# Kernel tuning notes

Measured on AMD Instinct MI355X. Metric: run time of the kernel, lower is better.

## Reference

```python
import jax, jax.numpy as jnp
import numpy as np

DIM = 1024
NUM_HEADS = 16
HEAD_DIM = DIM // NUM_HEADS


def setup_inputs() -> dict:
    key = jax.random.key(0)
    ks = jax.random.split(key, 6)
    B, N, C = 2, 2048, DIM
    s = 1.0 / np.sqrt(C)
    return {
        "x": jax.random.normal(ks[0], (B, N, C), dtype=jnp.float32),
        "Wq": jax.random.normal(ks[1], (C, C), dtype=jnp.float32) * s,
        "Wk": jax.random.normal(ks[2], (C, C), dtype=jnp.float32) * s,
        "Wv": jax.random.normal(ks[3], (C, C), dtype=jnp.float32) * s,
        "Wproj": jax.random.normal(ks[4], (C, C), dtype=jnp.float32) * s,
        "bproj": jax.random.normal(ks[5], (C,), dtype=jnp.float32) * 0.01,
    }


def reference(x, Wq, Wk, Wv, Wproj, bproj):
    B, N, C = x.shape
    H, D = NUM_HEADS, HEAD_DIM
    scale = D ** -0.5
    # Linear (torch convention: y = x @ W.T), then split heads -> [B, H, N, D]
    q = (x @ Wq.T).reshape(B, N, H, D).transpose(0, 2, 1, 3)
    k = (x @ Wk.T).reshape(B, N, H, D).transpose(0, 2, 1, 3)
    v = (x @ Wv.T).reshape(B, N, H, D).transpose(0, 2, 1, 3)
    attn = jnp.einsum("bhnd,bhmd->bhnm", q, k) * scale  # [B,H,N,N]
    attn = jax.nn.softmax(attn, axis=-1)
    out = jnp.einsum("bhnm,bhmd->bhnd", attn, v)  # [B,H,N,D]
    out = out.transpose(0, 2, 1, 3).reshape(B, N, C)
    return out @ Wproj.T + bproj
```

## Files before the change

kernel.cpp:

```cpp
#include <hip/hip_runtime.h>
#include <stdint.h>

typedef unsigned short u16;
typedef unsigned int u32;

typedef __bf16 bf16x8 __attribute__((ext_vector_type(8)));
typedef float f32x4 __attribute__((ext_vector_type(4)));

#define LOG2E_SCALE 0.18033688011112042f

static __device__ __forceinline__ u16 f2bf(float f) {
  union { float f; u32 u; } v; v.f = f;
  u32 r = v.u + 0x7fffu + ((v.u >> 16) & 1u);
  return (u16)(r >> 16);
}
static __device__ __forceinline__ u32 pk2(float a, float b) {
  u32 r;
  asm("v_cvt_pk_bf16_f32 %0, %1, %2" : "=v"(r) : "v"(a), "v"(b));
  return r;
}
static __device__ __forceinline__ float fexp2(float x) {
  return __builtin_amdgcn_exp2f(x);
}
static __device__ __forceinline__ float blo(u32 u) {
  union { u32 u; float f; } v; v.u = u << 16; return v.f;
}
static __device__ __forceinline__ float bhi(u32 u) {
  union { u32 u; float f; } v; v.u = u & 0xffff0000u; return v.f;
}

static __device__ __forceinline__ void gl_lds16(const void* g, void* l) {
  __builtin_amdgcn_global_load_lds(
      (const __attribute__((address_space(1))) u32*)g,
      (__attribute__((address_space(3))) u32*)l, 16, 0, 0);
}

__global__ void cast_kernel(const float* __restrict__ x, const float* __restrict__ wq,
                            const float* __restrict__ wk, const float* __restrict__ wv,
                            const float* __restrict__ wp,
                            u16* __restrict__ xb, u16* __restrict__ wqb, u16* __restrict__ wkb,
                            u16* __restrict__ wvb, u16* __restrict__ wpb) {
  const float* src; u16* dst; int n;
  switch (blockIdx.y) {
    case 0: src = x;  dst = xb;  n = 4194304; break;
    case 1: src = wq; dst = wqb; n = 1048576; break;
    case 2: src = wk; dst = wkb; n = 1048576; break;
    case 3: src = wv; dst = wvb; n = 1048576; break;
    default: src = wp; dst = wpb; n = 1048576; break;
  }
  int i = (blockIdx.x * 256 + threadIdx.x) * 8;
  if (i >= n) return;
  float4 a = *(const float4*)(src + i);
  float4 b = *(const float4*)(src + i + 4);
  uint4 o;
  o.x = pk2(a.x, a.y); o.y = pk2(a.z, a.w);
  o.z = pk2(b.x, b.y); o.w = pk2(b.z, b.w);
  *(uint4*)(dst + i) = o;
}

__global__ __launch_bounds__(256, 3) void gemm_qkv(
    const u16* __restrict__ A, const u16* __restrict__ Bq, const u16* __restrict__ Bk,
    const u16* __restrict__ Bv, u16* __restrict__ oQ, u16* __restrict__ oK,
    u16* __restrict__ oVt)
{
  constexpr int K = 1024;
  __shared__ u16 As[128 * 32];
  __shared__ u16 Bs[128 * 32];
  __shared__ float tbuf[4][16 * 68];

  const int tid  = threadIdx.x;
  const int lane = tid & 63;
  const int wave = tid >> 6;
  const int cl   = lane & 15;
  const int g    = lane >> 4;
  const int wm   = (wave >> 1) * 64;
  const int wn   = (wave & 1) * 64;
  const int bm   = blockIdx.y * 128;
  const int bn   = blockIdx.x * 128;
  const int z    = blockIdx.z;
  const u16* B = (z == 0 ? Bq : (z == 1 ? Bk : Bv));

  f32x4 zero4 = {0.f, 0.f, 0.f, 0.f};
  f32x4 acc[4][4];
#pragma unroll
  for (int i = 0; i < 4; i++)
#pragma unroll
    for (int j = 0; j < 4; j++) acc[i][j] = zero4;

  const int srow = tid >> 2;
  const int sch  = (tid & 3) ^ ((srow >> 1) & 3);
  const char* aG = (const char*)(A + (size_t)(bm + srow) * K) + sch * 16;
  const char* bG = (const char*)(B + (size_t)(bn + srow) * K) + sch * 16;
  char* aL = (char*)As + tid * 16;
  char* bL = (char*)Bs + tid * 16;
  const size_t rstep = (size_t)64 * K * 2;

  const int swz = (cl >> 1) & 3;

  for (int k0 = 0; k0 < K; k0 += 32) {
    gl_lds16(aG + k0 * 2, aL);
    gl_lds16(aG + rstep + k0 * 2, aL + 4096);
    gl_lds16(bG + k0 * 2, bL);
    gl_lds16(bG + rstep + k0 * 2, bL + 4096);
    __syncthreads();

    bf16x8 af[4], bf[4];
#pragma unroll
    for (int i = 0; i < 4; i++)
      af[i] = *(const bf16x8*)(As + (wm + i * 16 + cl) * 32 + ((g ^ swz) & 3) * 8);
#pragma unroll
    for (int j = 0; j < 4; j++)
      bf[j] = *(const bf16x8*)(Bs + (wn + j * 16 + cl) * 32 + ((g ^ swz) & 3) * 8);
#pragma unroll
    for (int i = 0; i < 4; i++)
#pragma unroll
      for (int j = 0; j < 4; j++)
        acc[i][j] = __builtin_amdgcn_mfma_f32_16x16x32_bf16(af[i], bf[j], acc[i][j], 0, 0, 0);
    __syncthreads();
  }

  const int rq = g * 4;
  if (z <= 1) {
    u16* o = z ? oK : oQ;
    const float cs = z ? 1.0f : LOG2E_SCALE;
#pragma unroll
    for (int i = 0; i < 4; i++)
#pragma unroll
      for (int j = 0; j < 4; j++)
#pragma unroll
        for (int r = 0; r < 4; r++) {
          int gm = bm + wm + i * 16 + rq + r;
          int gn = bn + wn + j * 16 + cl;
          int b = gm >> 11, ns = gm & 2047;
          int h = gn >> 6,  d  = gn & 63;
          o[(((size_t)(b * 16 + h)) * 2048 + ns) * 64 + d] = f2bf(acc[i][j][r] * cs);
        }
  } else {
    float* tb = tbuf[wave];
#pragma unroll
    for (int j = 0; j < 4; j++) {
      asm volatile("s_waitcnt lgkmcnt(0)" ::: "memory");
#pragma unroll
      for (int i = 0; i < 4; i++)
        *(f32x4*)(tb + cl * 68 + i * 16 + rq) = acc[i][j];
      asm volatile("s_waitcnt lgkmcnt(0)" ::: "memory");
#pragma unroll
      for (int half = 0; half < 2; half++) {
        int dd = lane >> 2, p = (lane & 3) + half * 4;
        f32x4 x0 = *(const f32x4*)(tb + dd * 68 + p * 8);
        f32x4 x1 = *(const f32x4*)(tb + dd * 68 + p * 8 + 4);
        uint4 pkd;
        pkd.x = pk2(x0[0], x0[1]); pkd.y = pk2(x0[2], x0[3]);
        pkd.z = pk2(x1[0], x1[1]); pkd.w = pk2(x1[2], x1[3]);
        int gn = bn + wn + j * 16 + dd;
        int gm = bm + wm + p * 8;
        int b = gm >> 11, nn = gm & 2047;
        int h = gn >> 6,  dl = gn & 63;
        *(uint4*)(oVt + (((size_t)(b * 16 + h)) * 64 + dl) * 2048 + nn) = pkd;
      }
    }
  }
}

__global__ __launch_bounds__(512, 6) void attn_kernel(
    const u16* __restrict__ Q, const u16* __restrict__ Km,
    const u16* __restrict__ Vt, u16* __restrict__ Op, float* __restrict__ lp)
{
  __shared__ u16 ks[2][64 * 64];
  __shared__ u16 vs[2][64 * 64];
  __shared__ u16 ps[128 * 36];

  const int tid  = threadIdx.x;
  const int lane = tid & 63;
  const int W    = tid >> 6;
  const int cl   = lane & 15;
  const int g    = lane >> 4;
  const int bh   = blockIdx.x;
  const int qt   = blockIdx.y;
  const int sp   = blockIdx.z;

  const char* kS = (const char*)Km + (size_t)bh * 2048 * 128 + (size_t)sp * 1024 * 128;
  const char* vS = (const char*)Vt + (size_t)bh * 64 * 4096 + (size_t)sp * 2048;

  const u16* qbase = Q + ((size_t)bh * 2048 + qt * 128 + W * 16) * 64;
  bf16x8 qf[2];
#pragma unroll
  for (int h = 0; h < 2; h++)
    qf[h] = *(const bf16x8*)(qbase + cl * 64 + h * 32 + g * 8);

  auto stage_k = [&](int t) {
    const char* kT = kS + (size_t)t * 8192;
    int kv = tid >> 3, s = tid & 7;
    gl_lds16(kT + kv * 128 + (((s ^ kv) & 7) * 16), (char*)ks[t & 1] + tid * 16);
  };
  auto stage_v = [&](int t) {
    const char* vT = vS + (size_t)t * 128;
    int d = tid >> 3, s = tid & 7;
    gl_lds16(vT + (size_t)d * 4096 + (((s ^ d) & 7) * 16), (char*)vs[t & 1] + tid * 16);
  };

  stage_k(0);
  stage_v(0);

  f32x4 zero4 = {0.f, 0.f, 0.f, 0.f};
  f32x4 o_acc[4];
#pragma unroll
  for (int j = 0; j < 4; j++) o_acc[j] = zero4;
  float li = 0.f;

  for (int t = 0; t < 16; ++t) {
    __syncthreads();
    if (t < 15) { stage_k(t + 1); stage_v(t + 1); }

    const u16* kb = ks[t & 1];
    const u16* vb = vs[t & 1];

    f32x4 st[4];
#pragma unroll
    for (int j = 0; j < 4; j++) st[j] = zero4;
#pragma unroll
    for (int h = 0; h < 2; h++) {
#pragma unroll
      for (int j = 0; j < 4; j++) {
        bf16x8 kf = *(const bf16x8*)(kb + (j * 16 + cl) * 64 + (((h * 4 + g) ^ (cl & 7)) & 7) * 8);
        st[j] = __builtin_amdgcn_mfma_f32_16x16x32_bf16(kf, qf[h], st[j], 0, 0, 0);
      }
    }

#pragma unroll
    for (int j = 0; j < 4; j++)
#pragma unroll
      for (int r = 0; r < 4; r++) {
        float p = fexp2(st[j][r]);
        st[j][r] = p;
        li += p;
      }

    char* prow = (char*)ps + (W * 16 + cl) * 72;
#pragma unroll
    for (int h32 = 0; h32 < 2; h32++) {
#pragma unroll
      for (int jj = 0; jj < 2; jj++) {
        int j = h32 * 2 + jj;
        uint2 w;
        w.x = pk2(st[j][0], st[j][1]);
        w.y = pk2(st[j][2], st[j][3]);
        *(uint2*)(prow + jj * 32 + g * 8) = w;
      }
      bf16x8 pf, vf[4];
      union { bf16x8 v; uint2 u[2]; } pu;
      pu.u[0] = *(const uint2*)(prow + g * 16);
      pu.u[1] = *(const uint2*)(prow + g * 16 + 8);
      pf = pu.v;
#pragma unroll
      for (int j = 0; j < 4; j++)
        vf[j] = *(const bf16x8*)(vb + (j * 16 + cl) * 64 + (((h32 * 4 + g) ^ (cl & 7)) & 7) * 8);
#pragma unroll
      for (int j = 0; j < 4; j++)
        o_acc[j] = __builtin_amdgcn_mfma_f32_16x16x32_bf16(pf, vf[j], o_acc[j], 0, 0, 0);
    }
  }

  li += __shfl_xor(li, 16, 64);
  li += __shfl_xor(li, 32, 64);
  const int b = bh >> 4, hh = bh & 15;
  u16* Os = Op + (size_t)sp * 4194304;
  float* ls = lp + sp * 65536;
  if (g == 0) ls[bh * 2048 + qt * 128 + W * 16 + cl] = li;
#pragma unroll
  for (int r = 0; r < 4; r++) {
    int row = qt * 128 + W * 16 + g * 4 + r;
    u16* orow = Os + ((size_t)b * 2048 + row) * 1024 + hh * 64;
#pragma unroll
    for (int j = 0; j < 4; j++)
      orow[j * 16 + cl] = f2bf(o_acc[j][r]);
  }
}

__global__ void reduce_o(const u16* __restrict__ Op, const float* __restrict__ lp,
                         u16* __restrict__ Ow) {
  int t = blockIdx.x * 256 + threadIdx.x;
  int idx = t * 8;
  int b   = idx >> 21;
  int rem = idx & 2097151;
  int row = rem >> 10;
  int h   = (rem & 1023) >> 6;
  int lidx = (b * 16 + h) * 2048 + row;
  float inv = 1.0f / (lp[lidx] + lp[65536 + lidx]);
  uint4 a = *(const uint4*)(Op + idx);
  uint4 c = *(const uint4*)(Op + 4194304 + idx);
  uint4 o;
  o.x = pk2((blo(a.x) + blo(c.x)) * inv, (bhi(a.x) + bhi(c.x)) * inv);
  o.y = pk2((blo(a.y) + blo(c.y)) * inv, (bhi(a.y) + bhi(c.y)) * inv);
  o.z = pk2((blo(a.z) + blo(c.z)) * inv, (bhi(a.z) + bhi(c.z)) * inv);
  o.w = pk2((blo(a.w) + blo(c.w)) * inv, (bhi(a.w) + bhi(c.w)) * inv);
  *(uint4*)(Ow + idx) = o;
}

__global__ __launch_bounds__(256, 4) void proj_gemm(
    const u16* __restrict__ A, const u16* __restrict__ B,
    float* __restrict__ out, const float* __restrict__ bias)
{
  constexpr int K = 1024;
  __shared__ u16 As[64 * 32];
  __shared__ u16 Bs[128 * 32];

  const int tid  = threadIdx.x;
  const int lane = tid & 63;
  const int wave = tid >> 6;
  const int cl   = lane & 15;
  const int g    = lane >> 4;
  const int wm   = (wave >> 1) * 32;
  const int wn   = (wave & 1) * 64;
  const int bm   = blockIdx.y * 64;
  const int bn   = blockIdx.x * 128;

  f32x4 zero4 = {0.f, 0.f, 0.f, 0.f};
  f32x4 acc[2][4];
#pragma unroll
  for (int i = 0; i < 2; i++)
#pragma unroll
    for (int j = 0; j < 4; j++) acc[i][j] = zero4;

  const int srow = tid >> 2;
  const int sch  = (tid & 3) ^ ((srow >> 1) & 3);
  const char* aG = (const char*)(A + (size_t)(bm + srow) * K) + sch * 16;
  const char* bG = (const char*)(B + (size_t)(bn + srow) * K) + sch * 16;
  char* aL = (char*)As + tid * 16;
  char* bL = (char*)Bs + tid * 16;
  const size_t rstep = (size_t)64 * K * 2;

  const int swz = (cl >> 1) & 3;

  for (int k0 = 0; k0 < K; k0 += 32) {
    gl_lds16(aG + k0 * 2, aL);
    gl_lds16(bG + k0 * 2, bL);
    gl_lds16(bG + rstep + k0 * 2, bL + 4096);
    __syncthreads();

    bf16x8 af[2], bf[4];
#pragma unroll
    for (int i = 0; i < 2; i++)
      af[i] = *(const bf16x8*)(As + (wm + i * 16 + cl) * 32 + ((g ^ swz) & 3) * 8);
#pragma unroll
    for (int j = 0; j < 4; j++)
      bf[j] = *(const bf16x8*)(Bs + (wn + j * 16 + cl) * 32 + ((g ^ swz) & 3) * 8);
#pragma unroll
    for (int i = 0; i < 2; i++)
#pragma unroll
      for (int j = 0; j < 4; j++)
        acc[i][j] = __builtin_amdgcn_mfma_f32_16x16x32_bf16(af[i], bf[j], acc[i][j], 0, 0, 0);
    __syncthreads();
  }

  const int rq = g * 4;
#pragma unroll
  for (int i = 0; i < 2; i++)
#pragma unroll
    for (int j = 0; j < 4; j++)
#pragma unroll
      for (int r = 0; r < 4; r++) {
        int gm = bm + wm + i * 16 + rq + r;
        int gn = bn + wn + j * 16 + cl;
        out[(size_t)gm * 1024 + gn] = acc[i][j][r] + bias[gn];
      }
}

extern "C" void kernel_launch(void* const* d_in, const int* in_sizes, int n_in,
                              void* d_out, int out_size, void* d_ws, size_t ws_size,
                              hipStream_t stream) {
  const float* x     = (const float*)d_in[0];
  const float* Wq    = (const float*)d_in[1];
  const float* Wk    = (const float*)d_in[2];
  const float* Wv    = (const float*)d_in[3];
  const float* Wp    = (const float*)d_in[4];
  const float* bproj = (const float*)d_in[5];

  u16* ws  = (u16*)d_ws;
  u16* xb  = ws;
  u16* wqb = xb + 4194304;
  u16* wkb = wqb + 1048576;
  u16* wvb = wkb + 1048576;
  u16* wpb = wvb + 1048576;
  u16* Qw  = wpb + 1048576;
  u16* Kw  = Qw + 4194304;
  u16* Vw  = Kw + 4194304;
  u16* Ow  = Vw + 4194304;
  u16* Opart = Ow + 4194304;
  float* lpart = (float*)(Opart + 8388608);
  (void)in_sizes; (void)n_in; (void)out_size; (void)ws_size;

  cast_kernel<<<dim3(2048, 5), 256, 0, stream>>>(x, Wq, Wk, Wv, Wp, xb, wqb, wkb, wvb, wpb);
  gemm_qkv<<<dim3(8, 32, 3), 256, 0, stream>>>(xb, wqb, wkb, wvb, Qw, Kw, Vw);
  attn_kernel<<<dim3(32, 16, 2), 512, 0, stream>>>(Qw, Kw, Vw, Opart, lpart);
  reduce_o<<<dim3(2048), 256, 0, stream>>>(Opart, lpart, Ow);
  proj_gemm<<<dim3(8, 64), 256, 0, stream>>>(Ow, wpb, (float*)d_out, bproj);
}
```

Measured before the change: 183.9 us.

## Fuse split-KV reduction into projection GEMM, double-buffer GEMMs, MFMA row sums

The reduce_o kernel is removed. The projection GEMM now loads both partial attention outputs plus their row sums while staging its A tile, and writes the normalized bf16 tile to LDS itself. This drops one launch and an intermediate round trip through memory. Both GEMMs get double-buffered LDS staging with one barrier per iteration, and the attention kernel computes row sums with an extra MFMA against a ones vector instead of scalar adds and shuffles. The cast kernel launch is compacted to remove idle blocks. The cost is that the partial reduction is recomputed by each of the 8 column blocks, and the A loads become register-routed rather than direct-to-LDS.

```diff
diff --git a/kernel.cpp b/kernel.cpp
--- a/kernel.cpp
+++ b/kernel.cpp
@@ -40,16 +40,21 @@
                             const float* __restrict__ wp,
                             u16* __restrict__ xb, u16* __restrict__ wqb, u16* __restrict__ wkb,
                             u16* __restrict__ wvb, u16* __restrict__ wpb) {
-  const float* src; u16* dst; int n;
-  switch (blockIdx.y) {
-    case 0: src = x;  dst = xb;  n = 4194304; break;
-    case 1: src = wq; dst = wqb; n = 1048576; break;
-    case 2: src = wk; dst = wkb; n = 1048576; break;
-    case 3: src = wv; dst = wvb; n = 1048576; break;
-    default: src = wp; dst = wpb; n = 1048576; break;
-  }
-  int i = (blockIdx.x * 256 + threadIdx.x) * 8;
-  if (i >= n) return;
+  int id = blockIdx.x;
+  const float* src; u16* dst; int local;
+  if (id < 2048) {
+    src = x; dst = xb; local = id;
+  } else {
+    int w = (id - 2048) >> 9;
+    local = (id - 2048) & 511;
+    switch (w) {
+      case 0: src = wq; dst = wqb; break;
+      case 1: src = wk; dst = wkb; break;
+      case 2: src = wv; dst = wvb; break;
+      default: src = wp; dst = wpb; break;
+    }
+  }
+  int i = (local * 256 + threadIdx.x) * 8;
   float4 a = *(const float4*)(src + i);
   float4 b = *(const float4*)(src + i + 4);
   uint4 o;
@@ -64,9 +69,7 @@
     u16* __restrict__ oVt)
 {
   constexpr int K = 1024;
-  __shared__ u16 As[128 * 32];
-  __shared__ u16 Bs[128 * 32];
-  __shared__ float tbuf[4][16 * 68];
+  __shared__ u16 smem[2][2][128 * 32];
 
   const int tid  = threadIdx.x;
   const int lane = tid & 63;
@@ -91,32 +94,39 @@
   const int sch  = (tid & 3) ^ ((srow >> 1) & 3);
   const char* aG = (const char*)(A + (size_t)(bm + srow) * K) + sch * 16;
   const char* bG = (const char*)(B + (size_t)(bn + srow) * K) + sch * 16;
-  char* aL = (char*)As + tid * 16;
-  char* bL = (char*)Bs + tid * 16;
   const size_t rstep = (size_t)64 * K * 2;
 
+  auto stage = [&](int it) {
+    char* aL = (char*)smem[it & 1][0] + tid * 16;
+    char* bL = (char*)smem[it & 1][1] + tid * 16;
+    gl_lds16(aG + it * 64, aL);
+    gl_lds16(aG + it * 64 + rstep, aL + 4096);
+    gl_lds16(bG + it * 64, bL);
+    gl_lds16(bG + it * 64 + rstep, bL + 4096);
+  };
+
+  stage(0);
+
   const int swz = (cl >> 1) & 3;
 
-  for (int k0 = 0; k0 < K; k0 += 32) {
-    gl_lds16(aG + k0 * 2, aL);
-    gl_lds16(aG + rstep + k0 * 2, aL + 4096);
-    gl_lds16(bG + k0 * 2, bL);
-    gl_lds16(bG + rstep + k0 * 2, bL + 4096);
+  for (int it = 0; it < 32; ++it) {
     __syncthreads();
-
+    if (it < 31) stage(it + 1);
+
+    const u16* as = smem[it & 1][0];
+    const u16* bs = smem[it & 1][1];
     bf16x8 af[4], bf[4];
 #pragma unroll
     for (int i = 0; i < 4; i++)
-      af[i] = *(const bf16x8*)(As + (wm + i * 16 + cl) * 32 + ((g ^ swz) & 3) * 8);
+      af[i] = *(const bf16x8*)(as + (wm + i * 16 + cl) * 32 + ((g ^ swz) & 3) * 8);
 #pragma unroll
     for (int j = 0; j < 4; j++)
-      bf[j] = *(const bf16x8*)(Bs + (wn + j * 16 + cl) * 32 + ((g ^ swz) & 3) * 8);
+      bf[j] = *(const bf16x8*)(bs + (wn + j * 16 + cl) * 32 + ((g ^ swz) & 3) * 8);
 #pragma unroll
     for (int i = 0; i < 4; i++)
 #pragma unroll
       for (int j = 0; j < 4; j++)
         acc[i][j] = __builtin_amdgcn_mfma_f32_16x16x32_bf16(af[i], bf[j], acc[i][j], 0, 0, 0);
-    __syncthreads();
   }
 
   const int rq = g * 4;
@@ -136,7 +146,8 @@
           o[(((size_t)(b * 16 + h)) * 2048 + ns) * 64 + d] = f2bf(acc[i][j][r] * cs);
         }
   } else {
-    float* tb = tbuf[wave];
+    __syncthreads();
+    float* tb = (float*)smem + wave * (16 * 68);
 #pragma unroll
     for (int j = 0; j < 4; j++) {
       asm volatile("s_waitcnt lgkmcnt(0)" ::: "memory");
@@ -188,6 +199,11 @@
   for (int h = 0; h < 2; h++)
     qf[h] = *(const bf16x8*)(qbase + cl * 64 + h * 32 + g * 8);
 
+  union { bf16x8 v; u32 u[4]; } onesu;
+#pragma unroll
+  for (int k = 0; k < 4; k++) onesu.u[k] = 0x3f803f80u;
+  const bf16x8 onesf = onesu.v;
+
   auto stage_k = [&](int t) {
     const char* kT = kS + (size_t)t * 8192;
     int kv = tid >> 3, s = tid & 7;
@@ -206,7 +222,7 @@
   f32x4 o_acc[4];
 #pragma unroll
   for (int j = 0; j < 4; j++) o_acc[j] = zero4;
-  float li = 0.f;
+  f32x4 l_acc = zero4;
 
   for (int t = 0; t < 16; ++t) {
     __syncthreads();
@@ -230,11 +246,8 @@
 #pragma unroll
     for (int j = 0; j < 4; j++)
 #pragma unroll
-      for (int r = 0; r < 4; r++) {
-        float p = fexp2(st[j][r]);
-        st[j][r] = p;
-        li += p;
-      }
+      for (int r = 0; r < 4; r++)
+        st[j][r] = fexp2(st[j][r]);
 
     char* prow = (char*)ps + (W * 16 + cl) * 72;
 #pragma unroll
@@ -258,15 +271,18 @@
 #pragma unroll
       for (int j = 0; j < 4; j++)
         o_acc[j] = __builtin_amdgcn_mfma_f32_16x16x32_bf16(pf, vf[j], o_acc[j], 0, 0, 0);
+      l_acc = __builtin_amdgcn_mfma_f32_16x16x32_bf16(pf, onesf, l_acc, 0, 0, 0);
     }
   }
 
-  li += __shfl_xor(li, 16, 64);
-  li += __shfl_xor(li, 32, 64);
   const int b = bh >> 4, hh = bh & 15;
   u16* Os = Op + (size_t)sp * 4194304;
   float* ls = lp + sp * 65536;
-  if (g == 0) ls[bh * 2048 + qt * 128 + W * 16 + cl] = li;
+  if (cl == 0) {
+#pragma unroll
+    for (int r = 0; r < 4; r++)
+      ls[bh * 2048 + qt * 128 + W * 16 + g * 4 + r] = l_acc[r];
+  }
 #pragma unroll
   for (int r = 0; r < 4; r++) {
     int row = qt * 128 + W * 16 + g * 4 + r;
@@ -277,33 +293,13 @@
   }
 }
 
-__global__ void reduce_o(const u16* __restrict__ Op, const float* __restrict__ lp,
-                         u16* __restrict__ Ow) {
-  int t = blockIdx.x * 256 + threadIdx.x;
-  int idx = t * 8;
-  int b   = idx >> 21;
-  int rem = idx & 2097151;
-  int row = rem >> 10;
-  int h   = (rem & 1023) >> 6;
-  int lidx = (b * 16 + h) * 2048 + row;
-  float inv = 1.0f / (lp[lidx] + lp[65536 + lidx]);
-  uint4 a = *(const uint4*)(Op + idx);
-  uint4 c = *(const uint4*)(Op + 4194304 + idx);
-  uint4 o;
-  o.x = pk2((blo(a.x) + blo(c.x)) * inv, (bhi(a.x) + bhi(c.x)) * inv);
-  o.y = pk2((blo(a.y) + blo(c.y)) * inv, (bhi(a.y) + bhi(c.y)) * inv);
-  o.z = pk2((blo(a.z) + blo(c.z)) * inv, (bhi(a.z) + bhi(c.z)) * inv);
-  o.w = pk2((blo(a.w) + blo(c.w)) * inv, (bhi(a.w) + bhi(c.w)) * inv);
-  *(uint4*)(Ow + idx) = o;
-}
-
 __global__ __launch_bounds__(256, 4) void proj_gemm(
-    const u16* __restrict__ A, const u16* __restrict__ B,
-    float* __restrict__ out, const float* __restrict__ bias)
+    const u16* __restrict__ Op, const float* __restrict__ lp,
+    const u16* __restrict__ B, float* __restrict__ out, const float* __restrict__ bias)
 {
   constexpr int K = 1024;
-  __shared__ u16 As[64 * 32];
-  __shared__ u16 Bs[128 * 32];
+  __shared__ u16 As[2][64 * 32];
+  __shared__ u16 Bs[2][128 * 32];
 
   const int tid  = threadIdx.x;
   const int lane = tid & 63;
@@ -324,33 +320,51 @@
 
   const int srow = tid >> 2;
   const int sch  = (tid & 3) ^ ((srow >> 1) & 3);
-  const char* aG = (const char*)(A + (size_t)(bm + srow) * K) + sch * 16;
+  const int gmA  = bm + srow;
+  const int bA   = gmA >> 11, rowA = gmA & 2047;
+  const u16* aBase = Op + (size_t)gmA * 1024 + sch * 8;
   const char* bG = (const char*)(B + (size_t)(bn + srow) * K) + sch * 16;
-  char* aL = (char*)As + tid * 16;
-  char* bL = (char*)Bs + tid * 16;
   const size_t rstep = (size_t)64 * K * 2;
 
+  auto stage = [&](int it) {
+    char* bL = (char*)Bs[it & 1] + tid * 16;
+    gl_lds16(bG + it * 64, bL);
+    gl_lds16(bG + it * 64 + rstep, bL + 4096);
+    int col = it * 32 + sch * 8;
+    int lidx = (bA * 16 + (col >> 6)) * 2048 + rowA;
+    float inv = 1.0f / (lp[lidx] + lp[65536 + lidx]);
+    uint4 a0 = *(const uint4*)(aBase + it * 32);
+    uint4 a1 = *(const uint4*)(aBase + it * 32 + 4194304);
+    uint4 o;
+    o.x = pk2((blo(a0.x) + blo(a1.x)) * inv, (bhi(a0.x) + bhi(a1.x)) * inv);
+    o.y = pk2((blo(a0.y) + blo(a1.y)) * inv, (bhi(a0.y) + bhi(a1.y)) * inv);
+    o.z = pk2((blo(a0.z) + blo(a1.z)) * inv, (bhi(a0.z) + bhi(a1.z)) * inv);
+    o.w = pk2((blo(a0.w) + blo(a1.w)) * inv, (bhi(a0.w) + bhi(a1.w)) * inv);
+    *(uint4*)((char*)As[it & 1] + tid * 16) = o;
+  };
+
+  stage(0);
+
   const int swz = (cl >> 1) & 3;
 
-  for (int k0 = 0; k0 < K; k0 += 32) {
-    gl_lds16(aG + k0 * 2, aL);
-    gl_lds16(bG + k0 * 2, bL);
-    gl_lds16(bG + rstep + k0 * 2, bL + 4096);
+  for (int it = 0; it < 32; ++it) {
     __syncthreads();
-
+    if (it < 31) stage(it + 1);
+
+    const u16* as = As[it & 1];
+    const u16* bs = Bs[it & 1];
     bf16x8 af[2], bf[4];
 #pragma unroll
     for (int i = 0; i < 2; i++)
-      af[i] = *(const bf16x8*)(As + (wm + i * 16 + cl) * 32 + ((g ^ swz) & 3) * 8);
+      af[i] = *(const bf16x8*)(as + (wm + i * 16 + cl) * 32 + ((g ^ swz) & 3) * 8);
 #pragma unroll
     for (int j = 0; j < 4; j++)
-      bf[j] = *(const bf16x8*)(Bs + (wn + j * 16 + cl) * 32 + ((g ^ swz) & 3) * 8);
+      bf[j] = *(const bf16x8*)(bs + (wn + j * 16 + cl) * 32 + ((g ^ swz) & 3) * 8);
 #pragma unroll
     for (int i = 0; i < 2; i++)
 #pragma unroll
       for (int j = 0; j < 4; j++)
         acc[i][j] = __builtin_amdgcn_mfma_f32_16x16x32_bf16(af[i], bf[j], acc[i][j], 0, 0, 0);
-    __syncthreads();
   }
 
   const int rq = g * 4;
@@ -385,14 +399,12 @@
   u16* Qw  = wpb + 1048576;
   u16* Kw  = Qw + 4194304;
   u16* Vw  = Kw + 4194304;
-  u16* Ow  = Vw + 4194304;
-  u16* Opart = Ow + 4194304;
+  u16* Opart = Vw + 4194304;
   float* lpart = (float*)(Opart + 8388608);
   (void)in_sizes; (void)n_in; (void)out_size; (void)ws_size;
 
-  cast_kernel<<<dim3(2048, 5), 256, 0, stream>>>(x, Wq, Wk, Wv, Wp, xb, wqb, wkb, wvb, wpb);
+  cast_kernel<<<dim3(4096), 256, 0, stream>>>(x, Wq, Wk, Wv, Wp, xb, wqb, wkb, wvb, wpb);
   gemm_qkv<<<dim3(8, 32, 3), 256, 0, stream>>>(xb, wqb, wkb, wvb, Qw, Kw, Vw);
   attn_kernel<<<dim3(32, 16, 2), 512, 0, stream>>>(Qw, Kw, Vw, Opart, lpart);
-  reduce_o<<<dim3(2048), 256, 0, stream>>>(Opart, lpart, Ow);
-  proj_gemm<<<dim3(8, 64), 256, 0, stream>>>(Ow, wpb, (float*)d_out, bproj);
-}
+  proj_gemm<<<dim3(8, 64), 256, 0, stream>>>(Opart, lpart, wpb, (float*)d_out, bproj);
+}
```

New measurement: 185.6 us. About the same (+0.9%).
